# Kernel optimization log

Measured on AMD Instinct MI355X. Metric: run time of the kernel, lower is better.

Reference implementation:

```python
import jax, jax.numpy as jnp
import numpy as np

B, T, C, H = 2, 2048, 1024, 16
D = C // H
NEG = -1e9


def setup_inputs() -> dict:
    key = jax.random.key(0)
    ks = jax.random.split(key, 16)
    s = C ** -0.5
    hidden_states = jax.random.normal(ks[0], (B, T, C), dtype=jnp.float32)
    causal = jnp.tril(jnp.ones((T, T), dtype=bool))
    attention_mask = jnp.where(causal, 0.0, NEG).astype(jnp.float32)[None, None]
    p = lambda k, sh: jax.random.normal(k, sh, dtype=jnp.float32) * s
    return {
        "hidden_states": hidden_states,
        "attention_mask": attention_mask,
        "Wq": p(ks[1], (C, C)), "bq": jnp.zeros((C,), jnp.float32),
        "Wk": p(ks[2], (C, C)), "bk": jnp.zeros((C,), jnp.float32),
        "Wv": p(ks[3], (C, C)), "bv": jnp.zeros((C,), jnp.float32),
        "Wo": p(ks[4], (C, C)), "bo": jnp.zeros((C,), jnp.float32),
        "Wr1": p(ks[5], (C, C)), "br1": jnp.zeros((C,), jnp.float32),
        "Wr2": p(ks[6], (C, 3)), "br2": jnp.zeros((3,), jnp.float32),
    }


def reference(hidden_states, attention_mask, Wq, bq, Wk, bk, Wv, bv, Wo, bo, Wr1, br1, Wr2, br2):
    b, t, c = hidden_states.shape
    scale = D ** -0.5
    q = (hidden_states @ Wq + bq).reshape(b, t, H, D)
    k = (hidden_states @ Wk + bk).reshape(b, t, H, D)
    v = (hidden_states @ Wv + bv).reshape(b, t, H, D)
    # dead-end routing MLP (gate_logits computed but unused in the original)
    gate_logits = jnp.tanh(hidden_states @ Wr1 + br1) @ Wr2 + br2
    lambdas = jax.nn.softmax(gate_logits, axis=-1)  # noqa: F841 (unused, faithful)
    # explicit (unfused) attention: [B,H,T,T] scores materialized
    scores = jnp.einsum("bqhd,bkhd->bhqk", q, k) * scale + attention_mask
    probs = jax.nn.softmax(scores, axis=-1)
    ctx = jnp.einsum("bhqk,bkhd->bqhd", probs, v).reshape(b, t, c)
    return ctx @ Wo + bo
```

## Files before the change

### kernel.cpp

```cpp
#include <hip/hip_runtime.h>
#include <hip/hip_fp16.h>
#include <math.h>

#define BDIM 2
#define TDIM 2048
#define CDIM 1024
#define HDIM 16
#define DDIM 64

typedef _Float16 f16x8 __attribute__((ext_vector_type(8)));
typedef _Float16 f16x4 __attribute__((ext_vector_type(4)));
typedef float f32x4 __attribute__((ext_vector_type(4)));

#define GLL16(gsrc, ldst)                                                      \
  __builtin_amdgcn_global_load_lds(                                            \
      (const __attribute__((address_space(1))) unsigned int*)(gsrc),           \
      (__attribute__((address_space(3))) unsigned int*)(ldst), 16, 0, 0)

#define SWZ(row) ((((row)&7) ^ (((row) >> 3) & 7)) << 4)

#define SCALE_LOG2E 0.1803368801111204f

__global__ __launch_bounds__(256) void cvt_f16(const float* __restrict__ in,
                                               __half* __restrict__ out,
                                               int n8) {
  int i = blockIdx.x * blockDim.x + threadIdx.x;
  if (i >= n8) return;
  const float4* p = (const float4*)in + (size_t)i * 2;
  float4 a = p[0], b = p[1];
  __half2* o = (__half2*)out + (size_t)i * 4;
  o[0] = __floats2half2_rn(a.x, a.y);
  o[1] = __floats2half2_rn(a.z, a.w);
  o[2] = __floats2half2_rn(b.x, b.y);
  o[3] = __floats2half2_rn(b.z, b.w);
}

__global__ __launch_bounds__(256) void transpose_cvt(
    const float* __restrict__ w0, const float* __restrict__ w1,
    const float* __restrict__ w2, const float* __restrict__ w3,
    __half* __restrict__ o0, __half* __restrict__ o1, __half* __restrict__ o2,
    __half* __restrict__ o3) {
  const float* src;
  __half* dst;
  switch (blockIdx.z) {
    case 0: src = w0; dst = o0; break;
    case 1: src = w1; dst = o1; break;
    case 2: src = w2; dst = o2; break;
    default: src = w3; dst = o3; break;
  }
  __shared__ float t[32][33];
  const int tx = threadIdx.x & 31, ty = threadIdx.x >> 5;
  const int k0 = blockIdx.y * 32, n0 = blockIdx.x * 32;
#pragma unroll
  for (int j = 0; j < 4; ++j)
    t[ty + j * 8][tx] = src[(size_t)(k0 + ty + j * 8) * CDIM + n0 + tx];
  __syncthreads();
#pragma unroll
  for (int j = 0; j < 4; ++j)
    dst[(size_t)(n0 + ty + j * 8) * CDIM + k0 + tx] =
        __float2half(t[tx][ty + j * 8]);
}

template <int NMAT, int OUT16>
__global__ __launch_bounds__(256) void gemm_f16_bt(
    const __half* __restrict__ A, const __half* __restrict__ Bt,
    const float* __restrict__ bias0, const float* __restrict__ bias1,
    const float* __restrict__ bias2, float* __restrict__ outf,
    __half* __restrict__ outh, int M, int K) {
  __shared__ _Float16 As[2][128][32];
  __shared__ _Float16 Bs[2][128][32];
  const int tid = threadIdx.x;
  const int wid = tid >> 6, lane = tid & 63;
  const int m0 = blockIdx.y * 128, n0 = blockIdx.x * 128;
  const int wr = (wid >> 1) * 64, wc = (wid & 1) * 64;
  const int srow = lane >> 2;
  const int scol = (lane & 3) * 8;

  const __half* asrc = A + (size_t)(m0 + wid * 32 + srow) * K + scol;
  const __half* bsrc = Bt + (size_t)(n0 + wid * 32 + srow) * K + scol;

  f32x4 acc[4][4] = {};
  const int NT = K / 32;

  GLL16(asrc, &As[0][wid * 32][0]);
  GLL16(asrc + 16 * K, &As[0][wid * 32 + 16][0]);
  GLL16(bsrc, &Bs[0][wid * 32][0]);
  GLL16(bsrc + 16 * K, &Bs[0][wid * 32 + 16][0]);
  __syncthreads();

  for (int t = 0; t < NT; ++t) {
    const int cur = t & 1;
    if (t + 1 < NT) {
      const int k0 = (t + 1) * 32;
      GLL16(asrc + k0, &As[cur ^ 1][wid * 32][0]);
      GLL16(asrc + k0 + 16 * K, &As[cur ^ 1][wid * 32 + 16][0]);
      GLL16(bsrc + k0, &Bs[cur ^ 1][wid * 32][0]);
      GLL16(bsrc + k0 + 16 * K, &Bs[cur ^ 1][wid * 32 + 16][0]);
    }
    f16x8 a[4], b[4];
#pragma unroll
    for (int m = 0; m < 4; ++m)
      a[m] =
          *(const f16x8*)&As[cur][wr + m * 16 + (lane & 15)][(lane >> 4) * 8];
#pragma unroll
    for (int n = 0; n < 4; ++n)
      b[n] =
          *(const f16x8*)&Bs[cur][wc + n * 16 + (lane & 15)][(lane >> 4) * 8];
#pragma unroll
    for (int m = 0; m < 4; ++m)
#pragma unroll
      for (int n = 0; n < 4; ++n)
        acc[m][n] = __builtin_amdgcn_mfma_f32_16x16x32_f16(a[m], b[n],
                                                           acc[m][n], 0, 0, 0);
    __syncthreads();
  }

  const float* bias = bias0;
  size_t obase = 0;
  int ncol0 = n0;
  if (NMAT == 3) {
    const int mat = n0 >> 10;
    bias = (mat == 0) ? bias0 : (mat == 1) ? bias1 : bias2;
    obase = (size_t)mat * ((size_t)M * CDIM);
    ncol0 = n0 & 1023;
  }
#pragma unroll
  for (int m = 0; m < 4; ++m)
#pragma unroll
    for (int n = 0; n < 4; ++n) {
      const int col = ncol0 + wc + n * 16 + (lane & 15);
      const float bb = bias[col];
#pragma unroll
      for (int j = 0; j < 4; ++j) {
        const int row = m0 + wr + m * 16 + (lane >> 4) * 4 + j;
        if (OUT16)
          outh[obase + (size_t)row * CDIM + col] =
              __float2half(acc[m][n][j] + bb);
        else
          outf[(size_t)row * CDIM + col] = acc[m][n][j] + bb;
      }
    }
}

__global__ __launch_bounds__(256) void attention_mfma(
    const __half* __restrict__ q, const __half* __restrict__ k,
    const __half* __restrict__ v, __half* __restrict__ ctx) {
  __shared__ _Float16 Kl[2][64][64];
  __shared__ _Float16 Vt[2][64][64];
  __shared__ _Float16 Pl[4][16][64];

  const int tid = threadIdx.x;
  const int wid = tid >> 6, lane = tid & 63;
  const int qt = (blockIdx.x + blockIdx.y) & 31;
  const int bh = blockIdx.y;
  const int b = bh >> 4, h = bh & 15;
  const int qbase = qt * 64;
  const int g = lane >> 4, r = lane & 15;

  const __half* qhead = q + ((size_t)b * TDIM) * CDIM + h * DDIM;
  const __half* khead = k + ((size_t)b * TDIM) * CDIM + h * DDIM;
  const __half* vhead = v + ((size_t)b * TDIM) * CDIM + h * DDIM;

  f16x8 qf[2];
  {
    const __half* qrow = qhead + (size_t)(qbase + wid * 16 + r) * CDIM;
    qf[0] = *(const f16x8*)(qrow + g * 8);
    qf[1] = *(const f16x8*)(qrow + g * 8 + 32);
  }

  const int vrow = tid >> 2, vcol = (tid & 3) * 16;
  const int kr8 = lane >> 3;
  const int c0 = wid * 2, c1 = wid * 2 + 1;
  const int kcol0 = (((lane & 7) ^ kr8 ^ c0) & 7) * 8;
  const int kcol1 = (((lane & 7) ^ kr8 ^ c1) & 7) * 8;

  f32x4 accT[4] = {};
  float m = -3.0e38f, l = 0.0f;

  const int nt = qt + 1;

  f16x8 va, vb;
  {
    const __half* vsrc = vhead + (size_t)vrow * CDIM + vcol;
    va = *(const f16x8*)(vsrc);
    vb = *(const f16x8*)(vsrc + 8);
    GLL16(khead + (size_t)(c0 * 8 + kr8) * CDIM + kcol0, &Kl[0][c0 * 8][0]);
    GLL16(khead + (size_t)(c1 * 8 + kr8) * CDIM + kcol1, &Kl[0][c1 * 8][0]);
  }
  asm volatile("s_waitcnt vmcnt(0)" ::: "memory");
  __builtin_amdgcn_sched_barrier(0);
  {
    char* vt0 = (char*)&Vt[0][0][0];
#pragma unroll
    for (int i = 0; i < 8; ++i) {
      const int d0 = vcol + i, d1 = vcol + 8 + i;
      *(_Float16*)(vt0 + d0 * 128 + ((vrow * 2) ^ SWZ(d0))) = va[i];
      *(_Float16*)(vt0 + d1 * 128 + ((vrow * 2) ^ SWZ(d1))) = vb[i];
    }
  }
  __syncthreads();

  for (int t = 0; t < nt; ++t) {
    const int cur = t & 1, nxt = cur ^ 1;
    if (t + 1 < nt) {
      const __half* vsrc = vhead + (size_t)((t + 1) * 64 + vrow) * CDIM + vcol;
      va = *(const f16x8*)(vsrc);
      vb = *(const f16x8*)(vsrc + 8);
      GLL16(khead + (size_t)((t + 1) * 64 + c0 * 8 + kr8) * CDIM + kcol0,
            &Kl[nxt][c0 * 8][0]);
      GLL16(khead + (size_t)((t + 1) * 64 + c1 * 8 + kr8) * CDIM + kcol1,
            &Kl[nxt][c1 * 8][0]);
    }

    f32x4 sT[4] = {};
    const char* klb = (const char*)&Kl[cur][0][0];
#pragma unroll
    for (int kk = 0; kk < 2; ++kk) {
#pragma unroll
      for (int kb = 0; kb < 4; ++kb) {
        const int krow = kb * 16 + r;
        f16x8 kf = *(const f16x8*)(klb + krow * 128 +
                                   ((g * 16 + kk * 64) ^ SWZ(krow)));
        sT[kb] =
            __builtin_amdgcn_mfma_f32_16x16x32_f16(kf, qf[kk], sT[kb], 0, 0, 0);
      }
    }

    const int qg = qbase + wid * 16 + r;
    if (t == qt) {
#pragma unroll
      for (int kb = 0; kb < 4; ++kb) {
        const int kg = t * 64 + kb * 16 + g * 4;
#pragma unroll
        for (int j = 0; j < 4; ++j)
          sT[kb][j] =
              (kg + j <= qg) ? sT[kb][j] * SCALE_LOG2E : -3.0e38f;
      }
    } else {
#pragma unroll
      for (int kb = 0; kb < 4; ++kb)
#pragma unroll
        for (int j = 0; j < 4; ++j) sT[kb][j] *= SCALE_LOG2E;
    }

    float mx = sT[0][0];
#pragma unroll
    for (int kb = 0; kb < 4; ++kb)
#pragma unroll
      for (int j = 0; j < 4; ++j) mx = fmaxf(mx, sT[kb][j]);
    mx = fmaxf(mx, __shfl_xor(mx, 16));
    mx = fmaxf(mx, __shfl_xor(mx, 32));
    const float mnew = fmaxf(m, mx);
    const float corr = exp2f(m - mnew);
    float psum = 0.f;
    float pv[4][4];
#pragma unroll
    for (int kb = 0; kb < 4; ++kb)
#pragma unroll
      for (int j = 0; j < 4; ++j) {
        pv[kb][j] = exp2f(sT[kb][j] - mnew);
        psum += pv[kb][j];
      }
    psum += __shfl_xor(psum, 16);
    psum += __shfl_xor(psum, 32);
    l = l * corr + psum;
    m = mnew;
#pragma unroll
    for (int n = 0; n < 4; ++n) accT[n] *= corr;

    char* pb = (char*)&Pl[wid][0][0];
#pragma unroll
    for (int kb = 0; kb < 4; ++kb) {
      f16x4 pq;
#pragma unroll
      for (int j = 0; j < 4; ++j) pq[j] = (_Float16)pv[kb][j];
      *(f16x4*)(pb + r * 128 + ((kb * 32 + g * 8) ^ SWZ(r))) = pq;
    }

    const char* vtb = (const char*)&Vt[cur][0][0];
#pragma unroll
    for (int kk = 0; kk < 2; ++kk) {
      f16x8 pa =
          *(const f16x8*)(pb + r * 128 + ((g * 16 + kk * 64) ^ SWZ(r)));
#pragma unroll
      for (int n = 0; n < 4; ++n) {
        const int vd = n * 16 + r;
        f16x8 vf =
            *(const f16x8*)(vtb + vd * 128 + ((g * 16 + kk * 64) ^ SWZ(vd)));
        accT[n] =
            __builtin_amdgcn_mfma_f32_16x16x32_f16(vf, pa, accT[n], 0, 0, 0);
      }
    }

    if (t + 1 < nt) {
      asm volatile("s_waitcnt vmcnt(2)" ::: "memory");
      __builtin_amdgcn_sched_barrier(0);
      char* vtn = (char*)&Vt[nxt][0][0];
#pragma unroll
      for (int i = 0; i < 8; ++i) {
        const int d0 = vcol + i, d1 = vcol + 8 + i;
        *(_Float16*)(vtn + d0 * 128 + ((vrow * 2) ^ SWZ(d0))) = va[i];
        *(_Float16*)(vtn + d1 * 128 + ((vrow * 2) ^ SWZ(d1))) = vb[i];
      }
    }
    __syncthreads();
  }

  const float inv = 1.0f / l;
  const int qg = qbase + wid * 16 + r;
  __half* orow = ctx + ((size_t)(b * TDIM + qg)) * CDIM + h * DDIM;
#pragma unroll
  for (int n = 0; n < 4; ++n) {
    f16x4 ov;
#pragma unroll
    for (int j = 0; j < 4; ++j) ov[j] = (_Float16)(accT[n][j] * inv);
    *(f16x4*)(orow + n * 16 + g * 4) = ov;
  }
}

extern "C" void kernel_launch(void* const* d_in, const int* in_sizes, int n_in,
                              void* d_out, int out_size, void* d_ws,
                              size_t ws_size, hipStream_t stream) {
  const float* hs = (const float*)d_in[0];
  const float* Wq = (const float*)d_in[2];
  const float* bq = (const float*)d_in[3];
  const float* Wk = (const float*)d_in[4];
  const float* bk = (const float*)d_in[5];
  const float* Wv = (const float*)d_in[6];
  const float* bv = (const float*)d_in[7];
  const float* Wo = (const float*)d_in[8];
  const float* bo = (const float*)d_in[9];
  float* out = (float*)d_out;

  const size_t NTOK = (size_t)BDIM * TDIM;
  const size_t NELEM = NTOK * CDIM;

  __half* q16 = (__half*)d_ws;
  __half* k16 = q16 + NELEM;
  __half* v16 = k16 + NELEM;
  __half* hs16 = v16 + NELEM;
  __half* ctx16 = hs16 + NELEM;
  __half* wqt = ctx16 + NELEM;
  __half* wkt = wqt + (size_t)CDIM * CDIM;
  __half* wvt = wkt + (size_t)CDIM * CDIM;
  __half* wot = wvt + (size_t)CDIM * CDIM;

  cvt_f16<<<dim3((NELEM / 8 + 255) / 256), dim3(256), 0, stream>>>(
      hs, hs16, (int)(NELEM / 8));
  transpose_cvt<<<dim3(32, 32, 4), dim3(256), 0, stream>>>(
      Wq, Wk, Wv, Wo, wqt, wkt, wvt, wot);

  dim3 gblk(256);
  gemm_f16_bt<3, 1><<<dim3(24, 32), gblk, 0, stream>>>(
      hs16, wqt, bq, bk, bv, nullptr, q16, (int)NTOK, CDIM);

  attention_mfma<<<dim3(TDIM / 64, BDIM * HDIM), dim3(256), 0, stream>>>(
      q16, k16, v16, ctx16);

  gemm_f16_bt<1, 0><<<dim3(8, 32), gblk, 0, stream>>>(
      ctx16, wot, bo, bo, bo, out, nullptr, (int)NTOK, CDIM);
}
```

Before: 258.1 us.

## Write V transposed from QKV GEMM and load it via direct-to-LDS in attention

The QKV GEMM epilogue now writes V in a transposed [C, tokens] layout, so the attention kernel can fill its V^T tile with global_load_lds and XOR swizzle. This replaces the register loads, scalar LDS transpose stores and explicit vmcnt waits. The GEMM also gains a BN template parameter, and the output projection uses 64-wide N tiles to double its block count from 256 to 512. The transposed V stores are 8-byte scattered writes with a token-count stride, which may cost some GEMM write efficiency.

```diff
diff --git a/kernel.cpp b/kernel.cpp
--- a/kernel.cpp
+++ b/kernel.cpp
@@ -61,31 +61,36 @@
         __float2half(t[tx][ty + j * 8]);
 }
 
-template <int NMAT, int OUT16>
+template <int NMAT, int OUT16, int BN>
 __global__ __launch_bounds__(256) void gemm_f16_bt(
     const __half* __restrict__ A, const __half* __restrict__ Bt,
     const float* __restrict__ bias0, const float* __restrict__ bias1,
     const float* __restrict__ bias2, float* __restrict__ outf,
     __half* __restrict__ outh, int M, int K) {
+  constexpr int NB = BN / 32;
+  constexpr int BG = BN / 64;
   __shared__ _Float16 As[2][128][32];
-  __shared__ _Float16 Bs[2][128][32];
+  __shared__ _Float16 Bs[2][BN][32];
   const int tid = threadIdx.x;
   const int wid = tid >> 6, lane = tid & 63;
-  const int m0 = blockIdx.y * 128, n0 = blockIdx.x * 128;
-  const int wr = (wid >> 1) * 64, wc = (wid & 1) * 64;
+  const int m0 = blockIdx.y * 128, n0 = blockIdx.x * BN;
+  const int wr = (wid >> 1) * 64, wc = (wid & 1) * (BN / 2);
   const int srow = lane >> 2;
   const int scol = (lane & 3) * 8;
 
   const __half* asrc = A + (size_t)(m0 + wid * 32 + srow) * K + scol;
-  const __half* bsrc = Bt + (size_t)(n0 + wid * 32 + srow) * K + scol;
-
-  f32x4 acc[4][4] = {};
+  const __half* bsrc = Bt + (size_t)(n0 + srow) * K + scol;
+
+  f32x4 acc[4][NB] = {};
   const int NT = K / 32;
 
   GLL16(asrc, &As[0][wid * 32][0]);
   GLL16(asrc + 16 * K, &As[0][wid * 32 + 16][0]);
-  GLL16(bsrc, &Bs[0][wid * 32][0]);
-  GLL16(bsrc + 16 * K, &Bs[0][wid * 32 + 16][0]);
+#pragma unroll
+  for (int i = 0; i < BG; ++i) {
+    const int row0 = wid * (16 * BG) + i * 16;
+    GLL16(bsrc + (size_t)row0 * K, &Bs[0][row0][0]);
+  }
   __syncthreads();
 
   for (int t = 0; t < NT; ++t) {
@@ -94,22 +99,25 @@
       const int k0 = (t + 1) * 32;
       GLL16(asrc + k0, &As[cur ^ 1][wid * 32][0]);
       GLL16(asrc + k0 + 16 * K, &As[cur ^ 1][wid * 32 + 16][0]);
-      GLL16(bsrc + k0, &Bs[cur ^ 1][wid * 32][0]);
-      GLL16(bsrc + k0 + 16 * K, &Bs[cur ^ 1][wid * 32 + 16][0]);
-    }
-    f16x8 a[4], b[4];
+#pragma unroll
+      for (int i = 0; i < BG; ++i) {
+        const int row0 = wid * (16 * BG) + i * 16;
+        GLL16(bsrc + (size_t)row0 * K + k0, &Bs[cur ^ 1][row0][0]);
+      }
+    }
+    f16x8 a[4], b[NB];
 #pragma unroll
     for (int m = 0; m < 4; ++m)
       a[m] =
           *(const f16x8*)&As[cur][wr + m * 16 + (lane & 15)][(lane >> 4) * 8];
 #pragma unroll
-    for (int n = 0; n < 4; ++n)
+    for (int n = 0; n < NB; ++n)
       b[n] =
           *(const f16x8*)&Bs[cur][wc + n * 16 + (lane & 15)][(lane >> 4) * 8];
 #pragma unroll
     for (int m = 0; m < 4; ++m)
 #pragma unroll
-      for (int n = 0; n < 4; ++n)
+      for (int n = 0; n < NB; ++n)
         acc[m][n] = __builtin_amdgcn_mfma_f32_16x16x32_f16(a[m], b[n],
                                                            acc[m][n], 0, 0, 0);
     __syncthreads();
@@ -118,33 +126,49 @@
   const float* bias = bias0;
   size_t obase = 0;
   int ncol0 = n0;
+  int mat = 0;
   if (NMAT == 3) {
-    const int mat = n0 >> 10;
+    mat = n0 >> 10;
     bias = (mat == 0) ? bias0 : (mat == 1) ? bias1 : bias2;
     obase = (size_t)mat * ((size_t)M * CDIM);
     ncol0 = n0 & 1023;
   }
-#pragma unroll
-  for (int m = 0; m < 4; ++m)
-#pragma unroll
-    for (int n = 0; n < 4; ++n) {
-      const int col = ncol0 + wc + n * 16 + (lane & 15);
-      const float bb = bias[col];
-#pragma unroll
-      for (int j = 0; j < 4; ++j) {
-        const int row = m0 + wr + m * 16 + (lane >> 4) * 4 + j;
-        if (OUT16)
-          outh[obase + (size_t)row * CDIM + col] =
-              __float2half(acc[m][n][j] + bb);
-        else
-          outf[(size_t)row * CDIM + col] = acc[m][n][j] + bb;
-      }
-    }
+  if (NMAT == 3 && mat == 2) {
+#pragma unroll
+    for (int m = 0; m < 4; ++m)
+#pragma unroll
+      for (int n = 0; n < NB; ++n) {
+        const int col = ncol0 + wc + n * 16 + (lane & 15);
+        const float bb = bias[col];
+        const int row0 = m0 + wr + m * 16 + (lane >> 4) * 4;
+        f16x4 qv;
+#pragma unroll
+        for (int j = 0; j < 4; ++j) qv[j] = (_Float16)(acc[m][n][j] + bb);
+        *(f16x4*)(outh + obase + (size_t)col * M + row0) = qv;
+      }
+  } else {
+#pragma unroll
+    for (int m = 0; m < 4; ++m)
+#pragma unroll
+      for (int n = 0; n < NB; ++n) {
+        const int col = ncol0 + wc + n * 16 + (lane & 15);
+        const float bb = bias[col];
+#pragma unroll
+        for (int j = 0; j < 4; ++j) {
+          const int row = m0 + wr + m * 16 + (lane >> 4) * 4 + j;
+          if (OUT16)
+            outh[obase + (size_t)row * CDIM + col] =
+                __float2half(acc[m][n][j] + bb);
+          else
+            outf[(size_t)row * CDIM + col] = acc[m][n][j] + bb;
+        }
+      }
+  }
 }
 
 __global__ __launch_bounds__(256) void attention_mfma(
     const __half* __restrict__ q, const __half* __restrict__ k,
-    const __half* __restrict__ v, __half* __restrict__ ctx) {
+    const __half* __restrict__ vT, __half* __restrict__ ctx) {
   __shared__ _Float16 Kl[2][64][64];
   __shared__ _Float16 Vt[2][64][64];
   __shared__ _Float16 Pl[4][16][64];
@@ -159,7 +183,8 @@
 
   const __half* qhead = q + ((size_t)b * TDIM) * CDIM + h * DDIM;
   const __half* khead = k + ((size_t)b * TDIM) * CDIM + h * DDIM;
-  const __half* vhead = v + ((size_t)b * TDIM) * CDIM + h * DDIM;
+  const size_t NTOK = (size_t)BDIM * TDIM;
+  const __half* vhead = vT + (size_t)(h * DDIM) * NTOK + (size_t)b * TDIM;
 
   f16x8 qf[2];
   {
@@ -168,48 +193,32 @@
     qf[1] = *(const f16x8*)(qrow + g * 8 + 32);
   }
 
-  const int vrow = tid >> 2, vcol = (tid & 3) * 16;
-  const int kr8 = lane >> 3;
+  const int r8 = lane >> 3;
   const int c0 = wid * 2, c1 = wid * 2 + 1;
-  const int kcol0 = (((lane & 7) ^ kr8 ^ c0) & 7) * 8;
-  const int kcol1 = (((lane & 7) ^ kr8 ^ c1) & 7) * 8;
+  const int col0 = (((lane & 7) ^ r8 ^ c0) & 7) * 8;
+  const int col1 = (((lane & 7) ^ r8 ^ c1) & 7) * 8;
 
   f32x4 accT[4] = {};
   float m = -3.0e38f, l = 0.0f;
 
   const int nt = qt + 1;
 
-  f16x8 va, vb;
-  {
-    const __half* vsrc = vhead + (size_t)vrow * CDIM + vcol;
-    va = *(const f16x8*)(vsrc);
-    vb = *(const f16x8*)(vsrc + 8);
-    GLL16(khead + (size_t)(c0 * 8 + kr8) * CDIM + kcol0, &Kl[0][c0 * 8][0]);
-    GLL16(khead + (size_t)(c1 * 8 + kr8) * CDIM + kcol1, &Kl[0][c1 * 8][0]);
-  }
-  asm volatile("s_waitcnt vmcnt(0)" ::: "memory");
-  __builtin_amdgcn_sched_barrier(0);
-  {
-    char* vt0 = (char*)&Vt[0][0][0];
-#pragma unroll
-    for (int i = 0; i < 8; ++i) {
-      const int d0 = vcol + i, d1 = vcol + 8 + i;
-      *(_Float16*)(vt0 + d0 * 128 + ((vrow * 2) ^ SWZ(d0))) = va[i];
-      *(_Float16*)(vt0 + d1 * 128 + ((vrow * 2) ^ SWZ(d1))) = vb[i];
-    }
-  }
+  GLL16(khead + (size_t)(c0 * 8 + r8) * CDIM + col0, &Kl[0][c0 * 8][0]);
+  GLL16(khead + (size_t)(c1 * 8 + r8) * CDIM + col1, &Kl[0][c1 * 8][0]);
+  GLL16(vhead + (size_t)(c0 * 8 + r8) * NTOK + col0, &Vt[0][c0 * 8][0]);
+  GLL16(vhead + (size_t)(c1 * 8 + r8) * NTOK + col1, &Vt[0][c1 * 8][0]);
   __syncthreads();
 
   for (int t = 0; t < nt; ++t) {
     const int cur = t & 1, nxt = cur ^ 1;
     if (t + 1 < nt) {
-      const __half* vsrc = vhead + (size_t)((t + 1) * 64 + vrow) * CDIM + vcol;
-      va = *(const f16x8*)(vsrc);
-      vb = *(const f16x8*)(vsrc + 8);
-      GLL16(khead + (size_t)((t + 1) * 64 + c0 * 8 + kr8) * CDIM + kcol0,
-            &Kl[nxt][c0 * 8][0]);
-      GLL16(khead + (size_t)((t + 1) * 64 + c1 * 8 + kr8) * CDIM + kcol1,
-            &Kl[nxt][c1 * 8][0]);
+      const size_t koff = (size_t)((t + 1) * 64);
+      GLL16(khead + (koff + c0 * 8 + r8) * CDIM + col0, &Kl[nxt][c0 * 8][0]);
+      GLL16(khead + (koff + c1 * 8 + r8) * CDIM + col1, &Kl[nxt][c1 * 8][0]);
+      GLL16(vhead + (size_t)(c0 * 8 + r8) * NTOK + koff + col0,
+            &Vt[nxt][c0 * 8][0]);
+      GLL16(vhead + (size_t)(c1 * 8 + r8) * NTOK + koff + col1,
+            &Vt[nxt][c1 * 8][0]);
     }
 
     f32x4 sT[4] = {};
@@ -233,8 +242,7 @@
         const int kg = t * 64 + kb * 16 + g * 4;
 #pragma unroll
         for (int j = 0; j < 4; ++j)
-          sT[kb][j] =
-              (kg + j <= qg) ? sT[kb][j] * SCALE_LOG2E : -3.0e38f;
+          sT[kb][j] = (kg + j <= qg) ? sT[kb][j] * SCALE_LOG2E : -3.0e38f;
       }
     } else {
 #pragma unroll
@@ -280,8 +288,7 @@
     const char* vtb = (const char*)&Vt[cur][0][0];
 #pragma unroll
     for (int kk = 0; kk < 2; ++kk) {
-      f16x8 pa =
-          *(const f16x8*)(pb + r * 128 + ((g * 16 + kk * 64) ^ SWZ(r)));
+      f16x8 pa = *(const f16x8*)(pb + r * 128 + ((g * 16 + kk * 64) ^ SWZ(r)));
 #pragma unroll
       for (int n = 0; n < 4; ++n) {
         const int vd = n * 16 + r;
@@ -289,18 +296,6 @@
             *(const f16x8*)(vtb + vd * 128 + ((g * 16 + kk * 64) ^ SWZ(vd)));
         accT[n] =
             __builtin_amdgcn_mfma_f32_16x16x32_f16(vf, pa, accT[n], 0, 0, 0);
-      }
-    }
-
-    if (t + 1 < nt) {
-      asm volatile("s_waitcnt vmcnt(2)" ::: "memory");
-      __builtin_amdgcn_sched_barrier(0);
-      char* vtn = (char*)&Vt[nxt][0][0];
-#pragma unroll
-      for (int i = 0; i < 8; ++i) {
-        const int d0 = vcol + i, d1 = vcol + 8 + i;
-        *(_Float16*)(vtn + d0 * 128 + ((vrow * 2) ^ SWZ(d0))) = va[i];
-        *(_Float16*)(vtn + d1 * 128 + ((vrow * 2) ^ SWZ(d1))) = vb[i];
       }
     }
     __syncthreads();
@@ -351,12 +346,12 @@
       Wq, Wk, Wv, Wo, wqt, wkt, wvt, wot);
 
   dim3 gblk(256);
-  gemm_f16_bt<3, 1><<<dim3(24, 32), gblk, 0, stream>>>(
+  gemm_f16_bt<3, 1, 128><<<dim3(24, 32), gblk, 0, stream>>>(
       hs16, wqt, bq, bk, bv, nullptr, q16, (int)NTOK, CDIM);
 
   attention_mfma<<<dim3(TDIM / 64, BDIM * HDIM), dim3(256), 0, stream>>>(
       q16, k16, v16, ctx16);
 
-  gemm_f16_bt<1, 0><<<dim3(8, 32), gblk, 0, stream>>>(
+  gemm_f16_bt<1, 0, 64><<<dim3(16, 32), gblk, 0, stream>>>(
       ctx16, wot, bo, bo, bo, out, nullptr, (int)NTOK, CDIM);
 }
```

New measurement: 283.5 us. 1.1x slower.
